# Performance work log

Measured on AMD Instinct MI355X. Metric: run time of the kernel, lower is better.

Reference implementation:

```python
import jax, jax.numpy as jnp
import numpy as np

VOCAB = 50000
WORD_DIM = 300
PAT_LEN = 6
DOC_LEN = 32768


def setup_inputs() -> dict:
    key = jax.random.key(0)
    k1, k2, k3, k4 = jax.random.split(key, 4)
    doc = jax.random.randint(k1, (DOC_LEN,), 0, VOCAB, dtype=jnp.int64)
    embeddings = jax.random.normal(k2, (VOCAB, WORD_DIM), dtype=jnp.float32)
    w = jax.random.normal(k3, (PAT_LEN, PAT_LEN, WORD_DIM), dtype=jnp.float32)
    # original code normalizes each w[i, j] to unit norm at init
    w = w / jnp.linalg.norm(w, axis=-1, keepdims=True)
    b = jax.random.normal(k4, (PAT_LEN, PAT_LEN), dtype=jnp.float32)
    return {"doc": doc, "embeddings": embeddings, "w": w, "b": b}


def reference(doc, embeddings, w, b):
    p = w.shape[0]
    # Only the superdiagonal (i, i+1) of the transition matrix is nonzero.
    idx = jnp.arange(p - 1)
    w_sd = w[idx, idx + 1]          # [p-1, d]
    b_sd = b[idx, idx + 1]          # [p-1]

    x = embeddings[doc]             # [T, d] embedding gather
    # vals[t, i] = sigmoid(w[i,i+1] . x_t + b[i,i+1])   -> [T, p-1]
    vals = jax.nn.sigmoid(x @ w_sd.T + b_sd)

    start = jnp.zeros((p,), dtype=vals.dtype).at[0].set(1.0)

    def step(hidden, v_t):
        # hidden @ T_t: new[j] = hidden[j-1] * vals[t, j-1] for j >= 1
        shifted = hidden[:-1] * v_t                       # [p-1]
        new_hidden = jnp.concatenate([jnp.zeros((1,), hidden.dtype), shifted]) + start
        return new_hidden, new_hidden[-1]                 # score contribution = hidden @ final

    _, contribs = jax.lax.scan(step, start, vals)
    return jnp.sum(contribs)
```

## Files before the change

kernel.cpp:

```cpp
#include <hip/hip_runtime.h>

#define T_LEN 32768
#define DIM   300
#define NCH   75
#define NP    5

__device__ __forceinline__ float fast_sigmoid(float z) {
    return 1.0f / (1.0f + __expf(-z));
}

__global__ __launch_bounds__(256, 8) void vals_kernel(
    const int*   __restrict__ doc,
    const float* __restrict__ emb,
    const float* __restrict__ w,
    const float* __restrict__ b,
    float*       __restrict__ vals)
{
    const int tid = threadIdx.x;
    const int g   = tid >> 4;
    const int sub = tid & 15;
    const int t   = blockIdx.x * 16 + g;

    const float* __restrict__ xrow = emb + (size_t)doc[t] * DIM;
    const float4 x0 = *reinterpret_cast<const float4*>(xrow + 4 * (sub));
    const float4 x1 = *reinterpret_cast<const float4*>(xrow + 4 * (sub + 16));
    const float4 x2 = *reinterpret_cast<const float4*>(xrow + 4 * (sub + 32));
    const float4 x3 = *reinterpret_cast<const float4*>(xrow + 4 * (sub + 48));
    float4 x4 = make_float4(0.f, 0.f, 0.f, 0.f);
    if (sub < NCH - 64)
        x4 = *reinterpret_cast<const float4*>(xrow + 4 * (sub + 64));

    float a0 = 0.f, a1 = 0.f, a2 = 0.f, a3 = 0.f, a4 = 0.f;

    #define ACC(xv, c)                                                                  \
        {                                                                               \
            const float4 w0 = *reinterpret_cast<const float4*>(w + 1  * DIM + 4 * (c)); \
            const float4 w1 = *reinterpret_cast<const float4*>(w + 8  * DIM + 4 * (c)); \
            const float4 w2 = *reinterpret_cast<const float4*>(w + 15 * DIM + 4 * (c)); \
            const float4 w3 = *reinterpret_cast<const float4*>(w + 22 * DIM + 4 * (c)); \
            const float4 w4 = *reinterpret_cast<const float4*>(w + 29 * DIM + 4 * (c)); \
            a0 += (xv).x * w0.x + (xv).y * w0.y + (xv).z * w0.z + (xv).w * w0.w;        \
            a1 += (xv).x * w1.x + (xv).y * w1.y + (xv).z * w1.z + (xv).w * w1.w;        \
            a2 += (xv).x * w2.x + (xv).y * w2.y + (xv).z * w2.z + (xv).w * w2.w;        \
            a3 += (xv).x * w3.x + (xv).y * w3.y + (xv).z * w3.z + (xv).w * w3.w;        \
            a4 += (xv).x * w4.x + (xv).y * w4.y + (xv).z * w4.z + (xv).w * w4.w;        \
        }
    ACC(x0, sub);
    ACC(x1, sub + 16);
    ACC(x2, sub + 32);
    ACC(x3, sub + 48);
    if (sub < NCH - 64) ACC(x4, sub + 64);
    #undef ACC

    #pragma unroll
    for (int off = 8; off >= 1; off >>= 1) {
        a0 += __shfl_xor(a0, off);
        a1 += __shfl_xor(a1, off);
        a2 += __shfl_xor(a2, off);
        a3 += __shfl_xor(a3, off);
        a4 += __shfl_xor(a4, off);
    }

    if (sub < NP) {
        const float a = (sub == 0) ? a0 : (sub == 1) ? a1 : (sub == 2) ? a2
                       : (sub == 3) ? a3 : a4;
        vals[sub * T_LEN + t] = fast_sigmoid(a + b[7 * sub + 1]);
    }
}

__global__ __launch_bounds__(256) void reduce_kernel(
    const float* __restrict__ vals,
    float*       __restrict__ out)
{
    const int s = blockIdx.x * 256 + threadIdx.x;
    float p = 0.f;
    if (s <= T_LEN - NP) {
        p = vals[s]
          * vals[1 * T_LEN + s + 1]
          * vals[2 * T_LEN + s + 2]
          * vals[3 * T_LEN + s + 3]
          * vals[4 * T_LEN + s + 4];
    }
    #pragma unroll
    for (int off = 32; off >= 1; off >>= 1) p += __shfl_xor(p, off);

    __shared__ float partial[4];
    if ((threadIdx.x & 63) == 0) partial[threadIdx.x >> 6] = p;
    __syncthreads();
    if (threadIdx.x == 0)
        atomicAdd(out, partial[0] + partial[1] + partial[2] + partial[3]);
}

extern "C" void kernel_launch(void* const* d_in, const int* in_sizes, int n_in,
                              void* d_out, int out_size, void* d_ws, size_t ws_size,
                              hipStream_t stream) {
    const int*   doc = (const int*)  d_in[0];
    const float* emb = (const float*)d_in[1];
    const float* w   = (const float*)d_in[2];
    const float* b   = (const float*)d_in[3];
    float*       out = (float*)d_out;
    float*       vals = (float*)d_ws;

    hipMemsetAsync(out, 0, sizeof(float), stream);

    vals_kernel<<<T_LEN / 16, 256, 0, stream>>>(doc, emb, w, b, vals);
    reduce_kernel<<<(T_LEN + 255) / 256, 256, 0, stream>>>(vals, out);
}
```

Before: 105.0 us.

## Fuse sigmoid computation with windowed product via overlapping LDS tiles

The vals computation and the 5-way diagonal product are merged into one kernel. Each block of 320 threads computes 20 rows (16 owned plus a 4-row halo) into LDS and forms per-block partial sums. A single-block kernel then sums the partials, which removes the global vals round trip, the memset and the atomic. The cost is 25% redundant gather and dot-product work for the halo rows.

```diff
diff --git a/kernel.cpp b/kernel.cpp
--- a/kernel.cpp
+++ b/kernel.cpp
@@ -4,24 +4,31 @@
 #define DIM   300
 #define NCH   75
 #define NP    5
+#define TB    16
+#define ROWS  20
+#define NBLK  (T_LEN / TB)
 
 __device__ __forceinline__ float fast_sigmoid(float z) {
     return 1.0f / (1.0f + __expf(-z));
 }
 
-__global__ __launch_bounds__(256, 8) void vals_kernel(
+__global__ __launch_bounds__(320, 8) void fused_block(
     const int*   __restrict__ doc,
     const float* __restrict__ emb,
     const float* __restrict__ w,
     const float* __restrict__ b,
-    float*       __restrict__ vals)
+    float*       __restrict__ partial)
 {
+    __shared__ float lds_v[ROWS][NP];
+
     const int tid = threadIdx.x;
     const int g   = tid >> 4;
     const int sub = tid & 15;
-    const int t   = blockIdx.x * 16 + g;
+    const int t0  = blockIdx.x * TB;
+    const int t   = t0 + g;
+    const int tc  = (t < T_LEN) ? t : (T_LEN - 1);
 
-    const float* __restrict__ xrow = emb + (size_t)doc[t] * DIM;
+    const float* __restrict__ xrow = emb + (size_t)doc[tc] * DIM;
     const float4 x0 = *reinterpret_cast<const float4*>(xrow + 4 * (sub));
     const float4 x1 = *reinterpret_cast<const float4*>(xrow + 4 * (sub + 16));
     const float4 x2 = *reinterpret_cast<const float4*>(xrow + 4 * (sub + 32));
@@ -64,31 +71,40 @@
     if (sub < NP) {
         const float a = (sub == 0) ? a0 : (sub == 1) ? a1 : (sub == 2) ? a2
                        : (sub == 3) ? a3 : a4;
-        vals[sub * T_LEN + t] = fast_sigmoid(a + b[7 * sub + 1]);
+        lds_v[g][sub] = fast_sigmoid(a + b[7 * sub + 1]);
+    }
+    __syncthreads();
+
+    if (tid < 64) {
+        float p = 0.f;
+        const int s = t0 + tid;
+        if (tid < TB && s <= T_LEN - NP) {
+            p = lds_v[tid + 0][0] * lds_v[tid + 1][1] * lds_v[tid + 2][2]
+              * lds_v[tid + 3][3] * lds_v[tid + 4][4];
+        }
+        #pragma unroll
+        for (int off = 32; off >= 1; off >>= 1) p += __shfl_xor(p, off);
+        if (tid == 0) partial[blockIdx.x] = p;
     }
 }
 
-__global__ __launch_bounds__(256) void reduce_kernel(
-    const float* __restrict__ vals,
+__global__ __launch_bounds__(256) void final_sum(
+    const float* __restrict__ partial,
     float*       __restrict__ out)
 {
-    const int s = blockIdx.x * 256 + threadIdx.x;
+    const int tid = threadIdx.x;
     float p = 0.f;
-    if (s <= T_LEN - NP) {
-        p = vals[s]
-          * vals[1 * T_LEN + s + 1]
-          * vals[2 * T_LEN + s + 2]
-          * vals[3 * T_LEN + s + 3]
-          * vals[4 * T_LEN + s + 4];
-    }
+    #pragma unroll
+    for (int k = 0; k < NBLK / 256; ++k)
+        p += partial[tid + 256 * k];
+
     #pragma unroll
     for (int off = 32; off >= 1; off >>= 1) p += __shfl_xor(p, off);
 
-    __shared__ float partial[4];
-    if ((threadIdx.x & 63) == 0) partial[threadIdx.x >> 6] = p;
+    __shared__ float ws[4];
+    if ((tid & 63) == 0) ws[tid >> 6] = p;
     __syncthreads();
-    if (threadIdx.x == 0)
-        atomicAdd(out, partial[0] + partial[1] + partial[2] + partial[3]);
+    if (tid == 0) out[0] = ws[0] + ws[1] + ws[2] + ws[3];
 }
 
 extern "C" void kernel_launch(void* const* d_in, const int* in_sizes, int n_in,
@@ -99,10 +115,8 @@
     const float* w   = (const float*)d_in[2];
     const float* b   = (const float*)d_in[3];
     float*       out = (float*)d_out;
-    float*       vals = (float*)d_ws;
+    float*       partial = (float*)d_ws;
 
-    hipMemsetAsync(out, 0, sizeof(float), stream);
-
-    vals_kernel<<<T_LEN / 16, 256, 0, stream>>>(doc, emb, w, b, vals);
-    reduce_kernel<<<(T_LEN + 255) / 256, 256, 0, stream>>>(vals, out);
+    fused_block<<<NBLK, 320, 0, stream>>>(doc, emb, w, b, partial);
+    final_sum<<<1, 256, 0, stream>>>(partial, out);
 }
```

New measurement: 106.0 us. No clear change (+1.0%).
